# Kernel tuning notes

Measured on AMD Instinct MI355X. Metric: run time of the kernel, lower is better.

Reference implementation:

```python
import jax, jax.numpy as jnp
import numpy as np

T, D, E = 16384, 4096, 64  # tokens, hidden dim, num experts


def setup_inputs() -> dict:
    key = jax.random.key(0)
    kx, kw = jax.random.split(key)
    x = jax.random.normal(kx, (T, D), dtype=jnp.float32)
    W = jax.random.normal(kw, (E, D), dtype=jnp.float32) * (1.0 / np.sqrt(D))
    b = jnp.zeros((E,), dtype=jnp.float32)
    return {"x": x, "W": W, "b": b}


def reference(x, W, b):
    # Linear: [T, D] @ [D, E] + [E] -> [T, E]
    logits = jnp.einsum("td,ed->te", x, W) + b
    probs = jax.nn.softmax(logits, axis=-1)
    # Top-2 selection over experts
    top2_vals, top2_idx = jax.lax.top_k(probs, 2)  # [T, 2]
    # Note: original applies softmax (not sum-renorm) to the top-2 probs
    norm2 = jax.nn.softmax(top2_vals, axis=-1)  # [T, 2]
    # Scatter back into a dense [T, E] gating distribution
    gating = jnp.zeros_like(probs)
    rows = jnp.arange(T)[:, None]
    gating = gating.at[rows, top2_idx].set(norm2)
    return gating
```

## Files before the change

kernel.cpp:

```cpp
#include <hip/hip_runtime.h>
#include <hip/hip_bf16.h>


typedef float  f32x4 __attribute__((ext_vector_type(4)));
typedef short  s16x8 __attribute__((ext_vector_type(8)));
typedef short  s16x4 __attribute__((ext_vector_type(4)));
typedef unsigned int u32;

#define T_TOK   16384
#define D_DIM   4096
#define E_EXP   64
#define KSPLIT  8
#define KSLICE  (D_DIM / KSPLIT)
#define KCHUNK  128
#define NCHUNK  (KSLICE / KCHUNK)
#define TAU     0.004f
#define WS_NEED (1024 * 1024 + 4 + 4 * T_TOK)

__device__ __forceinline__ unsigned short f2bf_rn(float f) {
    unsigned u = __builtin_bit_cast(unsigned, f);
    unsigned r = u + 0x7fffu + ((u >> 16) & 1u);
    return (unsigned short)(r >> 16);
}

__device__ __forceinline__ void gl16(const void* g, void* l) {
    __builtin_amdgcn_global_load_lds((const __attribute__((address_space(1))) u32*)g,
                                     (__attribute__((address_space(3))) u32*)l, 16, 0, 0);
}

__global__ __launch_bounds__(256)
void convw_kernel(const float* __restrict__ W, short* __restrict__ Whi, short* __restrict__ Wlo) {
    const int i = (blockIdx.x * 256 + threadIdx.x) * 4;
    f32x4 v = *(const f32x4*)(W + i);
    s16x4 h, l;
#pragma unroll
    for (int j = 0; j < 4; ++j) {
        unsigned short hb = f2bf_rn(v[j]);
        h[j] = (short)hb;
        float hf = __builtin_bit_cast(float, (unsigned)hb << 16);
        l[j] = (short)f2bf_rn(v[j] - hf);
    }
    *(s16x4*)(Whi + i) = h;
    *(s16x4*)(Wlo + i) = l;
}

__global__ __launch_bounds__(256, 2)
void gemm_logits(const float* __restrict__ x, const short* __restrict__ Whi,
                 const short* __restrict__ Wlo, float* __restrict__ out) {
    __shared__ __align__(16) short ldsb[2][2][64 * 128];
    const int lane = threadIdx.x & 63;
    const int wid  = threadIdx.x >> 6;
    const int r16  = lane & 15;
    const int q16  = lane >> 4;
    const int tb   = blockIdx.x * 256 + wid * 64;
    const int kbase = blockIdx.y * KSLICE;

    const float* ax[4];
#pragma unroll
    for (int m = 0; m < 4; ++m)
        ax[m] = x + (long)(tb + m * 16 + r16) * D_DIM + kbase + q16 * 8;

    f32x4 acc[4][4];
#pragma unroll
    for (int m = 0; m < 4; ++m)
#pragma unroll
        for (int n = 0; n < 4; ++n) acc[m][n] = (f32x4){0.f, 0.f, 0.f, 0.f};

#define STAGE(c_, bb_)                                                              \
    {                                                                               \
        _Pragma("unroll")                                                           \
        for (int r = 0; r < 4; ++r) {                                               \
            const int o  = wid * 4096 + r * 1024 + lane * 16;    \
            const int e  = o >> 8;                                                  \
            const int cs = (o & 255) ^ ((e & 7) << 4);         \
            const long gb = (long)e * (D_DIM * 2) + (long)(kbase + (c_)*KCHUNK) * 2 + cs; \
            const int lb = wid * 4096 + r * 1024;                                   \
            gl16((const char*)Whi + gb, (char*)&ldsb[bb_][0][0] + lb);              \
            gl16((const char*)Wlo + gb, (char*)&ldsb[bb_][1][0] + lb);              \
        }                                                                           \
    }

    STAGE(0, 0);
    __syncthreads();

#pragma unroll
    for (int c = 0; c < NCHUNK; ++c) {
        const int buf = c & 1;
        if (c + 1 < NCHUNK) STAGE(c + 1, buf ^ 1);

#pragma unroll
        for (int s = 0; s < 4; ++s) {
            const int ko = c * KCHUNK + s * 32;
            s16x8 ahi[4], alo[4];
#pragma unroll
            for (int m = 0; m < 4; ++m) {
                f32x4 a0 = *(const f32x4*)(ax[m] + ko);
                f32x4 a1 = *(const f32x4*)(ax[m] + ko + 4);
#pragma unroll
                for (int j = 0; j < 8; ++j) {
                    float f = (j < 4) ? a0[j] : a1[j - 4];
                    u32 u = __builtin_bit_cast(u32, f);
                    float hf = __builtin_bit_cast(float, u & 0xffff0000u);
                    ahi[m][j] = (short)(u >> 16);
                    alo[m][j] = (short)(__builtin_bit_cast(u32, f - hf) >> 16);
                }
            }
            const int crow = s * 64 + q16 * 16;
#pragma unroll
            for (int n = 0; n < 4; ++n) {
                const int e   = n * 16 + r16;
                const int off = e * 256 + (crow ^ ((e & 7) << 4));
                s16x8 bhi = *(const s16x8*)((const char*)&ldsb[buf][0][0] + off);
                s16x8 blo = *(const s16x8*)((const char*)&ldsb[buf][1][0] + off);
#pragma unroll
                for (int m = 0; m < 4; ++m) {
                    acc[m][n] = __builtin_amdgcn_mfma_f32_16x16x32_bf16(ahi[m], bhi, acc[m][n], 0, 0, 0);
                    acc[m][n] = __builtin_amdgcn_mfma_f32_16x16x32_bf16(alo[m], bhi, acc[m][n], 0, 0, 0);
                    acc[m][n] = __builtin_amdgcn_mfma_f32_16x16x32_bf16(ahi[m], blo, acc[m][n], 0, 0, 0);
                }
            }
        }
        __syncthreads();
    }

#pragma unroll
    for (int m = 0; m < 4; ++m) {
        const long rb = (long)(tb + m * 16 + q16 * 4);
#pragma unroll
        for (int n = 0; n < 4; ++n)
#pragma unroll
            for (int r = 0; r < 4; ++r)
                atomicAdd(out + (rb + r) * E_EXP + n * 16 + r16, acc[m][n][r]);
    }
#undef STAGE
}

__device__ __forceinline__ void argmax64(float& v, int& i) {
#pragma unroll
    for (int s = 32; s > 0; s >>= 1) {
        float ov = __shfl_xor(v, s);
        int   oi = __shfl_xor(i, s);
        if (ov > v || (ov == v && oi < i)) { v = ov; i = oi; }
    }
}

__device__ __forceinline__ float wave_gate_write(float l, int lane, float* __restrict__ outrow) {
    float v1 = l; int i1 = lane; argmax64(v1, i1);
    float v2 = (lane == i1) ? -INFINITY : l; int i2 = lane; argmax64(v2, i2);
    float v3 = (lane == i1 || lane == i2) ? -INFINITY : l; int i3 = lane; argmax64(v3, i3);
    (void)i3;

    float ex = __expf(l - v1);
    float Z = ex;
#pragma unroll
    for (int s = 32; s > 0; s >>= 1) Z += __shfl_xor(Z, s);

    float p1 = 1.0f / Z;
    float p2 = __expf(v2 - v1) / Z;
    float g1 = 1.0f / (1.0f + __expf(p2 - p1));
    float g2 = 1.0f / (1.0f + __expf(p1 - p2));

    outrow[lane] = (lane == i1) ? g1 : (lane == i2) ? g2 : 0.0f;
    return v2 - v3;
}

__global__ __launch_bounds__(256)
void finalize_router(float* __restrict__ out, const float* __restrict__ b,
                     int* __restrict__ flagc, int* __restrict__ flaglist) {
    const int lane = threadIdx.x & 63;
    const int t = blockIdx.x * 4 + (threadIdx.x >> 6);
    float l = out[(long)t * E_EXP + lane] + b[lane];
    float gap = wave_gate_write(l, lane, out + (long)t * E_EXP);
    if (gap < TAU && lane == 0) {
        int pos = atomicAdd(flagc, 1);
        flaglist[pos] = t;
    }
}

__device__ __forceinline__ void exact_row(const float* __restrict__ x, const float* __restrict__ W,
                                          const float* __restrict__ b, float* __restrict__ out,
                                          int t, int lane, int w, float (*lds)[64]) {
    const float* xr = x + (long)t * D_DIM + w * 1024;
    const float* wr = W + (long)lane * D_DIM + w * 1024;
    float acc = 0.f;
    for (int k = 0; k < 1024; k += 4) {
        f32x4 xv = *(const f32x4*)(xr + k);
        f32x4 wv = *(const f32x4*)(wr + k);
        acc += xv[0]*wv[0] + xv[1]*wv[1] + xv[2]*wv[2] + xv[3]*wv[3];
    }
    lds[w][lane] = acc;
    __syncthreads();
    if (w == 0) {
        float l = lds[0][lane] + lds[1][lane] + lds[2][lane] + lds[3][lane] + b[lane];
        wave_gate_write(l, lane, out + (long)t * E_EXP);
    }
    __syncthreads();
}

__global__ __launch_bounds__(256)
void fallback_exact(const float* __restrict__ x, const float* __restrict__ W,
                    const float* __restrict__ b, float* __restrict__ out,
                    const int* __restrict__ flags) {
    const int count = flags[0];
    const int lane = threadIdx.x & 63;
    const int w = threadIdx.x >> 6;
    __shared__ float lds[4][64];
    for (int fi = blockIdx.x; fi < count; fi += gridDim.x)
        exact_row(x, W, b, out, flags[1 + fi], lane, w, lds);
}

__global__ __launch_bounds__(256)
void exact_all(const float* __restrict__ x, const float* __restrict__ W,
               const float* __restrict__ b, float* __restrict__ out) {
    const int lane = threadIdx.x & 63;
    const int w = threadIdx.x >> 6;
    __shared__ float lds[4][64];
    for (int t = blockIdx.x; t < T_TOK; t += gridDim.x)
        exact_row(x, W, b, out, t, lane, w, lds);
}

extern "C" void kernel_launch(void* const* d_in, const int* in_sizes, int n_in,
                              void* d_out, int out_size, void* d_ws, size_t ws_size,
                              hipStream_t stream) {
    const float* x = (const float*)d_in[0];
    const float* W = (const float*)d_in[1];
    const float* b = (const float*)d_in[2];
    float* out = (float*)d_out;

    if (ws_size < (size_t)WS_NEED) {
        exact_all<<<2048, 256, 0, stream>>>(x, W, b, out);
        return;
    }

    char* ws = (char*)d_ws;
    short* Whi = (short*)ws;
    short* Wlo = (short*)(ws + 512 * 1024);
    int* flagc    = (int*)(ws + 1024 * 1024);
    int* flaglist = flagc + 1;

    hipMemsetAsync(out, 0, (size_t)T_TOK * E_EXP * sizeof(float), stream);
    hipMemsetAsync(flagc, 0, sizeof(int), stream);

    convw_kernel<<<256, 256, 0, stream>>>(W, Whi, Wlo);
    gemm_logits<<<dim3(T_TOK / 256, KSPLIT), 256, 0, stream>>>(x, Whi, Wlo, out);
    finalize_router<<<T_TOK / 4, 256, 0, stream>>>(out, b, flagc, flaglist);
    fallback_exact<<<1024, 256, 0, stream>>>(x, W, b, out, flagc);
}
```

Baseline: 477.7 us.

## Stage x through LDS via async loads and replace atomics with split-K partial buffers

The GEMM now stages activation tiles into per-wave LDS double buffers with global_load_lds and explicit vmcnt waits, instead of loading x directly into registers. It holds a 256-wide K chunk of W in LDS per subslice. KSPLIT drops from 8 to 4, and each split writes plain stores to its own partial buffer in the workspace instead of issuing atomicAdd on the output. The finalize kernel sums the four partials, and the output memset is removed. The cost is a much larger workspace (17 MB) and extra partial-buffer traffic, with fewer blocks and one block per CU, which may reduce latency hiding.

```diff
diff --git a/kernel.cpp b/kernel.cpp
--- a/kernel.cpp
+++ b/kernel.cpp
@@ -10,12 +10,12 @@
 #define T_TOK   16384
 #define D_DIM   4096
 #define E_EXP   64
-#define KSPLIT  8
+#define KSPLIT  4
 #define KSLICE  (D_DIM / KSPLIT)
-#define KCHUNK  128
-#define NCHUNK  (KSLICE / KCHUNK)
+#define SUBK    256
+#define KCHUNK  32
 #define TAU     0.004f
-#define WS_NEED (1024 * 1024 + 4 + 4 * T_TOK)
+#define WS_NEED (17 * 1024 * 1024 + 4 + 4 * T_TOK)
 
 __device__ __forceinline__ unsigned short f2bf_rn(float f) {
     unsigned u = __builtin_bit_cast(unsigned, f);
@@ -44,58 +44,74 @@
     *(s16x4*)(Wlo + i) = l;
 }
 
-__global__ __launch_bounds__(256, 2)
+__global__ __launch_bounds__(256, 1)
 void gemm_logits(const float* __restrict__ x, const short* __restrict__ Whi,
-                 const short* __restrict__ Wlo, float* __restrict__ out) {
-    __shared__ __align__(16) short ldsb[2][2][64 * 128];
+                 const short* __restrict__ Wlo, float* __restrict__ partial) {
+    __shared__ __align__(16) char Blds[2][64 * 512];
+    __shared__ __align__(16) char Alds[4][2][64 * 128];
     const int lane = threadIdx.x & 63;
     const int wid  = threadIdx.x >> 6;
     const int r16  = lane & 15;
     const int q16  = lane >> 4;
-    const int tb   = blockIdx.x * 256 + wid * 64;
+    const int wtb  = blockIdx.x * 256 + wid * 64;
     const int kbase = blockIdx.y * KSLICE;
 
-    const float* ax[4];
+    f32x4 acc[4][4];
 #pragma unroll
     for (int m = 0; m < 4; ++m)
-        ax[m] = x + (long)(tb + m * 16 + r16) * D_DIM + kbase + q16 * 8;
-
-    f32x4 acc[4][4];
-#pragma unroll
-    for (int m = 0; m < 4; ++m)
 #pragma unroll
         for (int n = 0; n < 4; ++n) acc[m][n] = (f32x4){0.f, 0.f, 0.f, 0.f};
 
-#define STAGE(c_, bb_)                                                              \
-    {                                                                               \
-        _Pragma("unroll")                                                           \
-        for (int r = 0; r < 4; ++r) {                                               \
-            const int o  = wid * 4096 + r * 1024 + lane * 16;    \
-            const int e  = o >> 8;                                                  \
-            const int cs = (o & 255) ^ ((e & 7) << 4);         \
-            const long gb = (long)e * (D_DIM * 2) + (long)(kbase + (c_)*KCHUNK) * 2 + cs; \
-            const int lb = wid * 4096 + r * 1024;                                   \
-            gl16((const char*)Whi + gb, (char*)&ldsb[bb_][0][0] + lb);              \
-            gl16((const char*)Wlo + gb, (char*)&ldsb[bb_][1][0] + lb);              \
-        }                                                                           \
-    }
-
-    STAGE(0, 0);
-    __syncthreads();
-
-#pragma unroll
-    for (int c = 0; c < NCHUNK; ++c) {
-        const int buf = c & 1;
-        if (c + 1 < NCHUNK) STAGE(c + 1, buf ^ 1);
-
-#pragma unroll
-        for (int s = 0; s < 4; ++s) {
-            const int ko = c * KCHUNK + s * 32;
+#define ASTAGE(buf_, kglob_)                                                         \
+    { _Pragma("unroll")                                                              \
+      for (int r = 0; r < 8; ++r) {                                                  \
+          const int o   = r * 1024 + lane * 16;                                      \
+          const int tok = o >> 7;                                                    \
+          const int scol = (o & 127) ^ ((tok & 7) << 4);                             \
+          gl16((const char*)(x + (long)(wtb + tok) * D_DIM + (kglob_)) + scol,       \
+               &Alds[wid][buf_][0] + r * 1024);                                      \
+      } }
+
+#define BSTAGE(kglob_)                                                               \
+    { _Pragma("unroll")                                                              \
+      for (int h = 0; h < 2; ++h) {                                                  \
+          const short* Wsrc = h ? Wlo : Whi;                                         \
+          _Pragma("unroll")                                                          \
+          for (int r = 0; r < 8; ++r) {                                              \
+              const int o = wid * 8192 + r * 1024 + lane * 16;                       \
+              const int e = o >> 9;                                                  \
+              const int scol = (o & 511) ^ ((e & 7) << 4);                           \
+              gl16((const char*)(Wsrc + (long)e * D_DIM + (kglob_)) + scol,          \
+                   &Blds[h][0] + wid * 8192 + r * 1024);                             \
+          } } }
+
+#pragma unroll 1
+    for (int ss = 0; ss < KSLICE / SUBK; ++ss) {
+        const int kss = kbase + ss * SUBK;
+        __syncthreads();
+        BSTAGE(kss);
+        ASTAGE(0, kss);
+        __syncthreads();
+
+#pragma unroll
+        for (int c = 0; c < SUBK / KCHUNK; ++c) {
+            const int buf = c & 1;
+            if (c < SUBK / KCHUNK - 1) {
+                ASTAGE(buf ^ 1, kss + (c + 1) * KCHUNK);
+                asm volatile("s_waitcnt vmcnt(8)" ::: "memory");
+            } else {
+                asm volatile("s_waitcnt vmcnt(0)" ::: "memory");
+            }
+            __builtin_amdgcn_sched_barrier(0);
+
             s16x8 ahi[4], alo[4];
 #pragma unroll
             for (int m = 0; m < 4; ++m) {
-                f32x4 a0 = *(const f32x4*)(ax[m] + ko);
-                f32x4 a1 = *(const f32x4*)(ax[m] + ko + 4);
+                const int tok = m * 16 + r16;
+                const char* ab = &Alds[wid][buf][0] + tok * 128;
+                const int sw = (tok & 7) << 4;
+                f32x4 a0 = *(const f32x4*)(ab + ((q16 * 32) ^ sw));
+                f32x4 a1 = *(const f32x4*)(ab + ((q16 * 32 + 16) ^ sw));
 #pragma unroll
                 for (int j = 0; j < 8; ++j) {
                     float f = (j < 4) ? a0[j] : a1[j - 4];
@@ -105,13 +121,13 @@
                     alo[m][j] = (short)(__builtin_bit_cast(u32, f - hf) >> 16);
                 }
             }
-            const int crow = s * 64 + q16 * 16;
+            const int bcol = c * 64 + q16 * 16;
 #pragma unroll
             for (int n = 0; n < 4; ++n) {
-                const int e   = n * 16 + r16;
-                const int off = e * 256 + (crow ^ ((e & 7) << 4));
-                s16x8 bhi = *(const s16x8*)((const char*)&ldsb[buf][0][0] + off);
-                s16x8 blo = *(const s16x8*)((const char*)&ldsb[buf][1][0] + off);
+                const int e = n * 16 + r16;
+                const int off = e * 512 + (bcol ^ ((e & 7) << 4));
+                s16x8 bhi = *(const s16x8*)(&Blds[0][0] + off);
+                s16x8 blo = *(const s16x8*)(&Blds[1][0] + off);
 #pragma unroll
                 for (int m = 0; m < 4; ++m) {
                     acc[m][n] = __builtin_amdgcn_mfma_f32_16x16x32_bf16(ahi[m], bhi, acc[m][n], 0, 0, 0);
@@ -120,19 +136,20 @@
                 }
             }
         }
-        __syncthreads();
-    }
-
+    }
+
+    float* Pk = partial + (long)blockIdx.y * T_TOK * E_EXP;
 #pragma unroll
     for (int m = 0; m < 4; ++m) {
-        const long rb = (long)(tb + m * 16 + q16 * 4);
+        const long rb = (long)(wtb + m * 16 + q16 * 4);
 #pragma unroll
         for (int n = 0; n < 4; ++n)
 #pragma unroll
-            for (int r = 0; r < 4; ++r)
-                atomicAdd(out + (rb + r) * E_EXP + n * 16 + r16, acc[m][n][r]);
-    }
-#undef STAGE
+            for (int j = 0; j < 4; ++j)
+                Pk[(rb + j) * E_EXP + n * 16 + r16] = acc[m][n][j];
+    }
+#undef ASTAGE
+#undef BSTAGE
 }
 
 __device__ __forceinline__ void argmax64(float& v, int& i) {
@@ -165,11 +182,15 @@
 }
 
 __global__ __launch_bounds__(256)
-void finalize_router(float* __restrict__ out, const float* __restrict__ b,
-                     int* __restrict__ flagc, int* __restrict__ flaglist) {
+void finalize_router(const float* __restrict__ part, const float* __restrict__ b,
+                     float* __restrict__ out, int* __restrict__ flagc,
+                     int* __restrict__ flaglist) {
     const int lane = threadIdx.x & 63;
     const int t = blockIdx.x * 4 + (threadIdx.x >> 6);
-    float l = out[(long)t * E_EXP + lane] + b[lane];
+    float l = b[lane];
+#pragma unroll
+    for (int ks = 0; ks < KSPLIT; ++ks)
+        l += part[(long)ks * T_TOK * E_EXP + (long)t * E_EXP + lane];
     float gap = wave_gate_write(l, lane, out + (long)t * E_EXP);
     if (gap < TAU && lane == 0) {
         int pos = atomicAdd(flagc, 1);
@@ -233,16 +254,16 @@
     }
 
     char* ws = (char*)d_ws;
-    short* Whi = (short*)ws;
-    short* Wlo = (short*)(ws + 512 * 1024);
-    int* flagc    = (int*)(ws + 1024 * 1024);
+    short* Whi    = (short*)ws;
+    short* Wlo    = (short*)(ws + 512 * 1024);
+    float* partial = (float*)(ws + 1024 * 1024);
+    int* flagc    = (int*)(ws + 17 * 1024 * 1024);
     int* flaglist = flagc + 1;
 
-    hipMemsetAsync(out, 0, (size_t)T_TOK * E_EXP * sizeof(float), stream);
     hipMemsetAsync(flagc, 0, sizeof(int), stream);
 
     convw_kernel<<<256, 256, 0, stream>>>(W, Whi, Wlo);
-    gemm_logits<<<dim3(T_TOK / 256, KSPLIT), 256, 0, stream>>>(x, Whi, Wlo, out);
-    finalize_router<<<T_TOK / 4, 256, 0, stream>>>(out, b, flagc, flaglist);
+    gemm_logits<<<dim3(T_TOK / 256, KSPLIT), 256, 0, stream>>>(x, Whi, Wlo, partial);
+    finalize_router<<<T_TOK / 4, 256, 0, stream>>>(partial, b, out, flagc, flaglist);
     fallback_exact<<<1024, 256, 0, stream>>>(x, W, b, out, flagc);
 }
```

Measured after the change: 491.3 us. 1.03x slower.
